# Kernel optimization log

Hardware: AMD Instinct MI355X
Metric: run time of the kernel (lower is better)

## Reference

```python
import jax, jax.numpy as jnp
import numpy as np

D = 512
HEADS, DIM_HEAD, LANDMARKS, PINV_ITERS = 8, 64, 256, 6
CONV_K = 33  # residual depthwise conv kernel over sequence dim


def _ln(x, g, b, eps=1e-5):
    mu = x.mean(-1, keepdims=True)
    var = ((x - mu) ** 2).mean(-1, keepdims=True)
    return (x - mu) / jnp.sqrt(var + eps) * g + b


def _moe(x, gw, gb, f1w, f1b, l1g, l1b, f2w, f2b, l2g, l2b, k):
    # Dense grouped-expert evaluation (same math as per-token dispatch in torch source).
    scores = x @ gw + gb                               # [B,N,E]
    topk_s, topk_i = jax.lax.top_k(scores, k)          # [B,N,k]
    h = jnp.einsum('bnd,edh->benh', x, f1w) + f1b[None, :, None, :]
    h = jax.nn.relu(_ln(h, l1g[None, :, None, :], l1b[None, :, None, :]))
    o = jnp.einsum('benh,ehd->bend', h, f2w) + f2b[None, :, None, :]
    o = _ln(o, l2g[None, :, None, :], l2b[None, :, None, :])  # [B,E,N,D]
    o = jnp.take_along_axis(jnp.swapaxes(o, 1, 2), topk_i[..., None], axis=2)  # [B,N,k,D]
    w = jax.nn.softmax(topk_s, axis=-1)[..., None]
    return (w * o).sum(axis=2) + x


def _pinv(x, iters):
    # Moore-Penrose iterative pseudoinverse (lucidrains nystrom-attention)
    col = jnp.abs(x).sum(-1).max()
    row = jnp.abs(x).sum(-2).max()
    z = jnp.swapaxes(x, -1, -2) / (col * row)
    I = jnp.eye(x.shape[-1], dtype=x.dtype)
    for _ in range(iters):
        xz = x @ z
        z = 0.25 * z @ (13 * I - xz @ (15 * I - xz @ (7 * I - xz)))
    return z


def _nystrom(x, qkv_w, out_w, out_b, conv_w):
    b, n, _ = x.shape
    m, h, dh = LANDMARKS, HEADS, DIM_HEAD
    pad = (m - n % m) % m
    x = jnp.pad(x, ((0, 0), (pad, 0), (0, 0)))  # pad at FRONT, as in source
    npd = n + pad
    qkv = x @ qkv_w                              # [b, npd, 3*h*dh]
    q, k, v = [t.reshape(b, npd, h, dh).transpose(0, 2, 1, 3) for t in jnp.split(qkv, 3, axis=-1)]
    q = q * dh ** -0.5
    l = npd // m
    q_l = q.reshape(b, h, m, l, dh).mean(3)      # landmark means
    k_l = k.reshape(b, h, m, l, dh).mean(3)
    attn1 = jax.nn.softmax(jnp.einsum('bhid,bhjd->bhij', q, k_l), -1)    # [b,h,npd,m]
    attn2 = jax.nn.softmax(jnp.einsum('bhid,bhjd->bhij', q_l, k_l), -1)  # [b,h,m,m]
    attn3 = jax.nn.softmax(jnp.einsum('bhid,bhjd->bhij', q_l, k), -1)    # [b,h,m,npd]
    out = (attn1 @ _pinv(attn2, PINV_ITERS)) @ (attn3 @ v)               # [b,h,npd,dh]
    res = jax.lax.conv_general_dilated(
        v, conv_w, (1, 1), [(CONV_K // 2, CONV_K // 2), (0, 0)],
        dimension_numbers=('NCHW', 'OIHW', 'NCHW'), feature_group_count=h)
    out = out + res
    out = out.transpose(0, 2, 1, 3).reshape(b, npd, h * dh)
    out = out @ out_w + out_b
    return out[:, -n:]


def setup_inputs() -> dict:
    key = jax.random.key(0)
    ks = iter(jax.random.split(key, 64))
    def rn(shape, s=0.02):
        return jax.random.normal(next(ks), shape, jnp.float32) * s
    inp = {'features': jax.random.normal(next(ks), (4, 6000, D), jnp.float32)}
    inp['cls_token'] = rn((1, 1, D), 1e-6)
    def moe_params(pfx, E):
        inp[pfx + '_gate_w'] = rn((D, E)); inp[pfx + '_gate_b'] = jnp.zeros((E,), jnp.float32)
        inp[pfx + '_fc1_w'] = rn((E, D, D)); inp[pfx + '_fc1_b'] = jnp.zeros((E, D), jnp.float32)
        inp[pfx + '_ln1_g'] = jnp.ones((E, D), jnp.float32); inp[pfx + '_ln1_b'] = jnp.zeros((E, D), jnp.float32)
        inp[pfx + '_fc2_w'] = rn((E, D, D)); inp[pfx + '_fc2_b'] = jnp.zeros((E, D), jnp.float32)
        inp[pfx + '_ln2_g'] = jnp.ones((E, D), jnp.float32); inp[pfx + '_ln2_b'] = jnp.zeros((E, D), jnp.float32)
    moe_params('moe1', 2)
    moe_params('moe2', 4)
    def layer_params(pfx):
        inp[pfx + '_norm_g'] = jnp.ones((D,), jnp.float32); inp[pfx + '_norm_b'] = jnp.zeros((D,), jnp.float32)
        inp[pfx + '_qkv_w'] = rn((D, 3 * HEADS * DIM_HEAD))
        inp[pfx + '_out_w'] = rn((HEADS * DIM_HEAD, D)); inp[pfx + '_out_b'] = jnp.zeros((D,), jnp.float32)
        inp[pfx + '_conv_w'] = rn((HEADS, 1, CONV_K, 1))
    layer_params('l1')
    layer_params('l2')
    return inp


def reference(features, cls_token,
              moe1_gate_w, moe1_gate_b, moe1_fc1_w, moe1_fc1_b, moe1_ln1_g, moe1_ln1_b, moe1_fc2_w, moe1_fc2_b, moe1_ln2_g, moe1_ln2_b,
              moe2_gate_w, moe2_gate_b, moe2_fc1_w, moe2_fc1_b, moe2_ln1_g, moe2_ln1_b, moe2_fc2_w, moe2_fc2_b, moe2_ln2_g, moe2_ln2_b,
              l1_norm_g, l1_norm_b, l1_qkv_w, l1_out_w, l1_out_b, l1_conv_w,
              l2_norm_g, l2_norm_b, l2_qkv_w, l2_out_w, l2_out_b, l2_conv_w):
    B, N, _ = features.shape
    _H = int(np.ceil(np.sqrt(N)))
    add = _H * _H - N
    h = jnp.concatenate([features, features[:, :add]], axis=1)      # square pad by wrap
    h = jnp.concatenate([jnp.broadcast_to(cls_token, (B, 1, D)), h], axis=1)
    h = _moe(h, moe1_gate_w, moe1_gate_b, moe1_fc1_w, moe1_fc1_b, moe1_ln1_g, moe1_ln1_b, moe1_fc2_w, moe1_fc2_b, moe1_ln2_g, moe1_ln2_b, k=1)
    h = h + _nystrom(_ln(h, l1_norm_g, l1_norm_b), l1_qkv_w, l1_out_w, l1_out_b, l1_conv_w)
    h = _moe(h, moe2_gate_w, moe2_gate_b, moe2_fc1_w, moe2_fc1_b, moe2_ln1_g, moe2_ln1_b, moe2_fc2_w, moe2_fc2_b, moe2_ln2_g, moe2_ln2_b, k=2)
    h = h + _nystrom(_ln(h, l2_norm_g, l2_norm_b), l2_qkv_w, l2_out_w, l2_out_b, l2_conv_w)
    return (h[:, 0], h[:, 1:])
```

## Files before the change

### kernel.cpp

```cpp
#include <hip/hip_runtime.h>
#include <hip/hip_bf16.h>

constexpr int BATCH = 4;
constexpr int NTOK  = 6085;
constexpr int BN_TOK = BATCH * NTOK;
constexpr int NPD   = 6144;
constexpr int RPAD  = BATCH * NPD;
constexpr int DMODEL = 512;
constexpr int NH = 8, DH = 64;
constexpr int NBH = BATCH * NH;
constexpr int LGRP = NPD / 256;
constexpr int PAD_FRONT = 59;
constexpr int CONVK = 33;
constexpr int NCH = 8;

typedef __attribute__((ext_vector_type(8))) short short8v;
typedef __attribute__((ext_vector_type(4))) float f32x4;

__device__ __forceinline__ unsigned short f2bf(float f) {
  unsigned u = __float_as_uint(f);
  u += 0x7FFF + ((u >> 16) & 1);
  return (unsigned short)(u >> 16);
}
__device__ __forceinline__ float bf2f(unsigned short h) {
  return __uint_as_float((unsigned)h << 16);
}


__global__ void k_build_h(const float* __restrict__ feat, const float* __restrict__ cls,
                          float* __restrict__ H) {
  size_t total = (size_t)BN_TOK * DMODEL;
  for (size_t idx = (size_t)blockIdx.x * blockDim.x + threadIdx.x; idx < total;
       idx += (size_t)gridDim.x * blockDim.x) {
    int d = (int)(idx & 511);
    size_t tok = idx >> 9;
    int b = (int)(tok / NTOK), n = (int)(tok % NTOK);
    float v;
    if (n == 0) v = cls[d];
    else {
      int i = n - 1; if (i >= 6000) i -= 6000;
      v = feat[((size_t)b * 6000 + i) * DMODEL + d];
    }
    H[idx] = v;
  }
}

__global__ void k_diag_fill(float* __restrict__ out, size_t n, float val) {
  for (size_t i = (size_t)blockIdx.x * blockDim.x + threadIdx.x; i < n;
       i += (size_t)gridDim.x * blockDim.x)
    out[i] = val;
}

__global__ __launch_bounds__(256) void k_wconv(const float* __restrict__ W, int ldb,
    unsigned short* __restrict__ hi, unsigned short* __restrict__ lo) {
  __shared__ unsigned short Th[64][80], Tl[64][80];
  int bk = blockIdx.y * 64, bn = blockIdx.x * 64;
  int t = threadIdx.x;
  int kr = t >> 2, cq = (t & 3) * 16;
  const float* src = W + (size_t)(bk + kr) * ldb + bn + cq;
  #pragma unroll
  for (int q = 0; q < 4; ++q) {
    float4 v = *(const float4*)(src + q * 4);
    float vs[4] = {v.x, v.y, v.z, v.w};
    #pragma unroll
    for (int e = 0; e < 4; ++e) {
      int n = cq + q * 4 + e;
      unsigned short h = f2bf(vs[e]);
      Th[n][kr] = h;
      Tl[n][kr] = f2bf(vs[e] - bf2f(h));
    }
  }
  __syncthreads();
  int nr = t >> 2, kq = (t & 3) * 16;
  size_t o = (size_t)(bn + nr) * 512 + bk + kq;
  *(short8v*)&hi[o]     = *(const short8v*)&Th[nr][kq];
  *(short8v*)&hi[o + 8] = *(const short8v*)&Th[nr][kq + 8];
  *(short8v*)&lo[o]     = *(const short8v*)&Tl[nr][kq];
  *(short8v*)&lo[o + 8] = *(const short8v*)&Tl[nr][kq + 8];
}

__global__ __launch_bounds__(256) void k_gemm_mfma(const float* __restrict__ A,
    const unsigned short* __restrict__ BtH, const unsigned short* __restrict__ BtL,
    const float* __restrict__ bias, float* __restrict__ C,
    int M, int lda, int ldc, float alpha, int omode)
{
  __shared__ unsigned short AsH[128][40], AsL[128][40];
  __shared__ unsigned short BsH[128][40], BsL[128][40];
  int bm = blockIdx.y * 128, bn = blockIdx.x * 128;
  int tid = threadIdx.x;
  int wave = tid >> 6, lane = tid & 63;
  int mo = (wave >> 1) * 64, no = (wave & 1) * 64;
  int r16 = lane & 15, g = lane >> 4;
  f32x4 acc[4][4] = {};
  int srow = tid >> 1, shalf = (tid & 1) * 16;
  const float* aptr = A + (size_t)(bm + srow) * lda + shalf;
  bool avalid = (bm + srow) < M;
  const unsigned short* bhptr = BtH + (size_t)(bn + srow) * 512 + shalf;
  const unsigned short* blptr = BtL + (size_t)(bn + srow) * 512 + shalf;
  for (int k0 = 0; k0 < 512; k0 += 32) {
    unsigned short h8[16], l8[16];
    #pragma unroll
    for (int q = 0; q < 4; ++q) {
      float4 v = avalid ? *(const float4*)(aptr + k0 + q * 4) : make_float4(0.f, 0.f, 0.f, 0.f);
      float vs[4] = {v.x, v.y, v.z, v.w};
      #pragma unroll
      for (int e = 0; e < 4; ++e) {
        unsigned short hh = f2bf(vs[e]);
        h8[q * 4 + e] = hh;
        l8[q * 4 + e] = f2bf(vs[e] - bf2f(hh));
      }
    }
    *(short8v*)&AsH[srow][shalf]     = *(short8v*)&h8[0];
    *(short8v*)&AsH[srow][shalf + 8] = *(short8v*)&h8[8];
    *(short8v*)&AsL[srow][shalf]     = *(short8v*)&l8[0];
    *(short8v*)&AsL[srow][shalf + 8] = *(short8v*)&l8[8];
    *(short8v*)&BsH[srow][shalf]     = *(const short8v*)(bhptr + k0);
    *(short8v*)&BsH[srow][shalf + 8] = *(const short8v*)(bhptr + k0 + 8);
    *(short8v*)&BsL[srow][shalf]     = *(const short8v*)(blptr + k0);
    *(short8v*)&BsL[srow][shalf + 8] = *(const short8v*)(blptr + k0 + 8);
    __syncthreads();
    short8v ah[4], al[4], bh[4], bl[4];
    #pragma unroll
    for (int mt = 0; mt < 4; ++mt) {
      ah[mt] = *(const short8v*)&AsH[mo + mt * 16 + r16][g * 8];
      al[mt] = *(const short8v*)&AsL[mo + mt * 16 + r16][g * 8];
    }
    #pragma unroll
    for (int nt = 0; nt < 4; ++nt) {
      bh[nt] = *(const short8v*)&BsH[no + nt * 16 + r16][g * 8];
      bl[nt] = *(const short8v*)&BsL[no + nt * 16 + r16][g * 8];
    }
    #pragma unroll
    for (int mt = 0; mt < 4; ++mt)
      #pragma unroll
      for (int nt = 0; nt < 4; ++nt) {
        acc[mt][nt] = __builtin_amdgcn_mfma_f32_16x16x32_bf16(ah[mt], bh[nt], acc[mt][nt], 0, 0, 0);
        acc[mt][nt] = __builtin_amdgcn_mfma_f32_16x16x32_bf16(ah[mt], bl[nt], acc[mt][nt], 0, 0, 0);
        acc[mt][nt] = __builtin_amdgcn_mfma_f32_16x16x32_bf16(al[mt], bh[nt], acc[mt][nt], 0, 0, 0);
      }
    __syncthreads();
  }
  #pragma unroll
  for (int mt = 0; mt < 4; ++mt)
    #pragma unroll
    for (int nt = 0; nt < 4; ++nt)
      #pragma unroll
      for (int j = 0; j < 4; ++j) {
        int gr = bm + mo + mt * 16 + g * 4 + j;
        int gc = bn + no + nt * 16 + r16;
        if (gr >= M) continue;
        float v = alpha * acc[mt][nt][j] + (bias ? bias[gc] : 0.f);
        if (omode == 0) {
          C[(size_t)gr * ldc + gc] = v;
        } else if (omode == 2) {
          int bb = gr / NPD, ii = gr % NPD;
          if (ii >= PAD_FRONT)
            C[((size_t)bb * NTOK + ii - PAD_FRONT) * 512 + gc] += v;
        } else {
          int bb = gr / NPD, ii = gr % NPD;
          int hh = gc >> 6, dd = gc & 63;
          C[(((size_t)bb * NH + hh) * NPD + ii) * 64 + dd] = v;
        }
      }
}

__global__ __launch_bounds__(256) void k_gemm(const float* __restrict__ A,
    const float* __restrict__ B,
    const float* __restrict__ bias, float* __restrict__ C,
    int M, int N, int K, int lda, int ldb, int ldc,
    long long sA, long long sB, long long sC, float alpha, int omode, float cdiag)
{
  __shared__ float As[16][65];
  __shared__ float Bs[16][65];
  int z = blockIdx.z;
  A += (size_t)z * (size_t)sA;
  B += (size_t)z * (size_t)sB;
  int bm = blockIdx.y * 64, bn = blockIdx.x * 64;
  int tid = threadIdx.x;
  int tr = tid >> 4, tc = tid & 15;
  int ar = tid >> 2, aq = tid & 3;
  int br = tid >> 4, bq = tid & 15;
  float acc[4][4] = {};
  for (int k0 = 0; k0 < K; k0 += 16) {
    {
      int gr = bm + ar;
      float4 v = make_float4(0.f, 0.f, 0.f, 0.f);
      if (gr < M) v = *(const float4*)&A[(size_t)gr * lda + k0 + aq * 4];
      As[aq * 4 + 0][ar] = v.x; As[aq * 4 + 1][ar] = v.y;
      As[aq * 4 + 2][ar] = v.z; As[aq * 4 + 3][ar] = v.w;
    }
    {
      float4 v = *(const float4*)&B[(size_t)(k0 + br) * ldb + bn + bq * 4];
      Bs[br][bq * 4 + 0] = v.x; Bs[br][bq * 4 + 1] = v.y;
      Bs[br][bq * 4 + 2] = v.z; Bs[br][bq * 4 + 3] = v.w;
    }
    __syncthreads();
    #pragma unroll
    for (int kk = 0; kk < 16; ++kk) {
      float a[4], bv[4];
      #pragma unroll
      for (int i = 0; i < 4; ++i) a[i] = As[kk][tr * 4 + i];
      #pragma unroll
      for (int j = 0; j < 4; ++j) bv[j] = Bs[kk][tc * 4 + j];
      #pragma unroll
      for (int i = 0; i < 4; ++i)
        #pragma unroll
        for (int j = 0; j < 4; ++j) acc[i][j] += a[i] * bv[j];
    }
    __syncthreads();
  }
  #pragma unroll
  for (int i = 0; i < 4; ++i) {
    int gr = bm + tr * 4 + i;
    if (gr >= M) continue;
    #pragma unroll
    for (int j = 0; j < 4; ++j) {
      int gc = bn + tc * 4 + j;
      float v;
      if (omode == 5) {
        v = ((gr == gc) ? cdiag : 0.f) - acc[i][j];
      } else {
        v = alpha * acc[i][j] + (bias ? bias[gc] : 0.f);
      }
      C[(size_t)z * (size_t)sC + (size_t)gr * ldc + gc] = v;
    }
  }
}

__global__ void k_gate(const float* __restrict__ X, const float* __restrict__ gw,
                       const float* __restrict__ gb, float* __restrict__ WT, int E, int k) {
  int tok = blockIdx.x; int lane = threadIdx.x;
  const float* x = X + (size_t)tok * DMODEL;
  float s[4] = {0.f, 0.f, 0.f, 0.f};
  for (int d = lane; d < DMODEL; d += 64) {
    float xv = x[d];
    for (int e = 0; e < E; ++e) s[e] += xv * gw[(size_t)d * E + e];
  }
  #pragma unroll
  for (int off = 32; off; off >>= 1) {
    #pragma unroll
    for (int e = 0; e < 4; ++e) s[e] += __shfl_down(s[e], off);
  }
  if (lane == 0) {
    for (int e = 0; e < E; ++e) s[e] += gb[e];
    float w[4] = {0.f, 0.f, 0.f, 0.f};
    int i1 = 0;
    for (int e = 1; e < E; ++e) if (s[e] > s[i1]) i1 = e;
    if (k == 1) {
      w[i1] = 1.f;
    } else {
      int i2 = -1;
      for (int e = 0; e < E; ++e) { if (e == i1) continue; if (i2 < 0 || s[e] > s[i2]) i2 = e; }
      float e2 = expf(s[i2] - s[i1]);
      float zz = 1.f + e2;
      w[i1] = 1.f / zz; w[i2] = e2 / zz;
    }
    #pragma unroll
    for (int e = 0; e < 4; ++e) WT[(size_t)tok * 4 + e] = w[e];
  }
}

__device__ __forceinline__ void wave_ln_stats(const float* x, int lane, float& mu, float& rstd) {
  float s = 0.f, q = 0.f;
  #pragma unroll
  for (int j = 0; j < 8; ++j) { float v = x[lane + 64 * j]; s += v; q += v * v; }
  #pragma unroll
  for (int off = 32; off; off >>= 1) { s += __shfl_xor(s, off); q += __shfl_xor(q, off); }
  mu = s * (1.f / 512.f);
  float var = q * (1.f / 512.f) - mu * mu;
  rstd = rsqrtf(var + 1e-5f);
}

__global__ void k_ln_relu(float* __restrict__ T, const float* __restrict__ g,
                          const float* __restrict__ b) {
  int row = blockIdx.x; int lane = threadIdx.x;
  float* x = T + (size_t)row * 512;
  float mu, rstd; wave_ln_stats(x, lane, mu, rstd);
  #pragma unroll
  for (int j = 0; j < 8; ++j) {
    int d = lane + 64 * j;
    float v = (x[d] - mu) * rstd * g[d] + b[d];
    x[d] = fmaxf(v, 0.f);
  }
}

__global__ void k_ln_waccum(const float* __restrict__ T, float* __restrict__ H,
                            const float* __restrict__ g, const float* __restrict__ b,
                            const float* __restrict__ WT, int e) {
  int row = blockIdx.x;
  float w = WT[(size_t)row * 4 + e];
  if (w == 0.f) return;
  int lane = threadIdx.x;
  const float* x = T + (size_t)row * 512;
  float mu, rstd; wave_ln_stats(x, lane, mu, rstd);
  float* h = H + (size_t)row * 512;
  #pragma unroll
  for (int j = 0; j < 8; ++j) {
    int d = lane + 64 * j;
    h[d] += w * ((x[d] - mu) * rstd * g[d] + b[d]);
  }
}

__global__ void k_ln_pad(const float* __restrict__ H, float* __restrict__ XLn,
                         const float* __restrict__ g, const float* __restrict__ b) {
  int row = blockIdx.x; int lane = threadIdx.x;
  int bb = row / NPD, i = row % NPD;
  float* y = XLn + (size_t)row * 512;
  if (i < PAD_FRONT) {
    #pragma unroll
    for (int j = 0; j < 8; ++j) y[lane + 64 * j] = 0.f;
    return;
  }
  const float* x = H + ((size_t)bb * NTOK + (i - PAD_FRONT)) * 512;
  float mu, rstd; wave_ln_stats(x, lane, mu, rstd);
  #pragma unroll
  for (int j = 0; j < 8; ++j) {
    int d = lane + 64 * j;
    y[d] = (x[d] - mu) * rstd * g[d] + b[d];
  }
}

__global__ void k_xmean(const float* __restrict__ XLn, float* __restrict__ Xm) {
  int z = blockIdx.x;
  int c = threadIdx.x;
  int b = z >> 8, jm = z & 255;
  const float* base = XLn + ((size_t)b * NPD + jm * LGRP) * 512 + c;
  float s = 0.f;
  #pragma unroll
  for (int t = 0; t < LGRP; ++t) s += base[(size_t)t * 512];
  Xm[(size_t)z * 512 + c] = s * (1.f / LGRP);
}

__global__ __launch_bounds__(256) void k_attn2(const float* __restrict__ QL,
                                               const float* __restrict__ KL,
                                               float* __restrict__ A2) {
  int z = blockIdx.x; int bh = z >> 8, j = z & 255;
  int b = bh >> 3, h = bh & 7;
  int t = threadIdx.x;
  __shared__ float q[64]; __shared__ float red[256];
  __shared__ float mshare, sshare;
  if (t < 64) q[t] = QL[((size_t)b * 256 + j) * 512 + h * 64 + t];
  __syncthreads();
  const float* kl = KL + ((size_t)b * 256 + t) * 512 + h * 64;
  float s = 0.f;
  #pragma unroll
  for (int d = 0; d < 64; ++d) s += q[d] * kl[d];
  red[t] = s; __syncthreads();
  for (int st = 128; st; st >>= 1) { if (t < st) red[t] = fmaxf(red[t], red[t + st]); __syncthreads(); }
  if (t == 0) mshare = red[0];
  __syncthreads();
  float e = expf(s - mshare);
  red[t] = e; __syncthreads();
  for (int st = 128; st; st >>= 1) { if (t < st) red[t] += red[t + st]; __syncthreads(); }
  if (t == 0) sshare = red[0];
  __syncthreads();
  A2[((size_t)bh * 256 + j) * 256 + t] = e / sshare;
}

__global__ __launch_bounds__(256) void k_pinv_scalars(const float* __restrict__ A2,
                                                      unsigned int* __restrict__ sc) {
  int bh = blockIdx.x; int t = threadIdx.x;
  const float* A = A2 + (size_t)bh * 65536;
  float rowsum = 0.f, colsum = 0.f;
  for (int jj = 0; jj < 256; ++jj) {
    rowsum += fabsf(A[(size_t)t * 256 + jj]);
    colsum += fabsf(A[(size_t)jj * 256 + t]);
  }
  __shared__ float sh[256];
  sh[t] = rowsum; __syncthreads();
  for (int s = 128; s; s >>= 1) { if (t < s) sh[t] = fmaxf(sh[t], sh[t + s]); __syncthreads(); }
  if (t == 0) atomicMax(&sc[0], __float_as_uint(sh[0]));
  __syncthreads();
  sh[t] = colsum; __syncthreads();
  for (int s = 128; s; s >>= 1) { if (t < s) sh[t] = fmaxf(sh[t], sh[t + s]); __syncthreads(); }
  if (t == 0) atomicMax(&sc[1], __float_as_uint(sh[0]));
}

__global__ void k_zinit(const float* __restrict__ A2, float* __restrict__ Z,
                        const unsigned int* __restrict__ sc) {
  float scale = 1.f / (__uint_as_float(sc[0]) * __uint_as_float(sc[1]));
  size_t total = (size_t)NBH * 65536;
  for (size_t idx = (size_t)blockIdx.x * blockDim.x + threadIdx.x; idx < total;
       idx += (size_t)gridDim.x * blockDim.x) {
    size_t bh = idx >> 16; int r = (int)((idx >> 8) & 255); int cc = (int)(idx & 255);
    Z[idx] = A2[(bh << 16) + (size_t)cc * 256 + r] * scale;
  }
}

__global__ void k_diagsub(const float* __restrict__ in, float* __restrict__ out, float cdiag) {
  size_t total = (size_t)NBH * 65536;
  for (size_t idx = (size_t)blockIdx.x * blockDim.x + threadIdx.x; idx < total;
       idx += (size_t)gridDim.x * blockDim.x) {
    int r = (int)((idx >> 8) & 255); int cc = (int)(idx & 255);
    out[idx] = ((r == cc) ? cdiag : 0.f) - in[idx];
  }
}

__global__ __launch_bounds__(256) void k_flash_mfma(
    const float* __restrict__ Qp, long long Qsb, long long Qsh, int Qsr,
    const float* __restrict__ Kp, long long Ksb, long long Ksh, int Ksr,
    const float* __restrict__ Vp, long long Vsb, long long Vsh, int Vsr,
    float* __restrict__ Op, long long Osb, long long Osh, int Osr,
    float* __restrict__ Opart, float* __restrict__ ML,
    int tiles_per_chunk, int mode)
{
  int jt = blockIdx.x, bh = blockIdx.y, ch = blockIdx.z;
  int b = bh >> 3, h = bh & 7;
  const float* Qb = Qp + (size_t)b * Qsb + (size_t)h * Qsh;
  const float* Kb = Kp + (size_t)b * Ksb + (size_t)h * Ksh;
  const float* Vb = Vp + (size_t)b * Vsb + (size_t)h * Vsh;
  int tid = threadIdx.x;
  int wave = tid >> 6, lane = tid & 63;
  int r16 = lane & 15, g = lane >> 4;
  int q0 = jt * 64 + wave * 16;

  __shared__ unsigned short KsH[64][72], KsL[64][72];
  __shared__ unsigned short VtH[64][72], VtL[64][72];

  short8v qh[2], ql[2];
  #pragma unroll
  for (int kk = 0; kk < 2; ++kk) {
    const float* qr = Qb + (size_t)(q0 + r16) * Qsr + kk * 32 + g * 8;
    float4 v0 = *(const float4*)qr;
    float4 v1 = *(const float4*)(qr + 4);
    float vs[8] = {v0.x, v0.y, v0.z, v0.w, v1.x, v1.y, v1.z, v1.w};
    unsigned short hh[8], llo[8];
    #pragma unroll
    for (int e = 0; e < 8; ++e) {
      hh[e] = f2bf(vs[e]); llo[e] = f2bf(vs[e] - bf2f(hh[e]));
    }
    qh[kk] = *(short8v*)&hh[0];
    ql[kk] = *(short8v*)&llo[0];
  }

  f32x4 O4[4] = {};
  float m[4], lsum[4];
  #pragma unroll
  for (int j = 0; j < 4; ++j) { m[j] = -1e30f; lsum[j] = 0.f; }

  int skey = tid >> 2, sq = (tid & 3) * 16;
  int t0 = ch * tiles_per_chunk;
  for (int tt = t0; tt < t0 + tiles_per_chunk; ++tt) {
    int key0 = tt * 64;
    __syncthreads();
    {
      const float* krow = Kb + (size_t)(key0 + skey) * Ksr + sq;
      const float* vrow = Vb + (size_t)(key0 + skey) * Vsr + sq;
      #pragma unroll
      for (int q = 0; q < 4; ++q) {
        float4 kv = *(const float4*)(krow + q * 4);
        float4 vv = *(const float4*)(vrow + q * 4);
        float ks[4] = {kv.x, kv.y, kv.z, kv.w};
        float vvs[4] = {vv.x, vv.y, vv.z, vv.w};
        #pragma unroll
        for (int e = 0; e < 4; ++e) {
          int d = sq + q * 4 + e;
          unsigned short khh = f2bf(ks[e]);
          KsH[skey][d] = khh;
          KsL[skey][d] = f2bf(ks[e] - bf2f(khh));
          unsigned short vhh = f2bf(vvs[e]);
          VtH[d][skey] = vhh;
          VtL[d][skey] = f2bf(vvs[e] - bf2f(vhh));
        }
      }
    }
    __syncthreads();
    f32x4 S[4] = {};
    #pragma unroll
    for (int kk = 0; kk < 2; ++kk)
      #pragma unroll
      for (int nt = 0; nt < 4; ++nt) {
        short8v kh = *(const short8v*)&KsH[nt * 16 + r16][kk * 32 + g * 8];
        short8v kl = *(const short8v*)&KsL[nt * 16 + r16][kk * 32 + g * 8];
        S[nt] = __builtin_amdgcn_mfma_f32_16x16x32_bf16(qh[kk], kh, S[nt], 0, 0, 0);
        S[nt] = __builtin_amdgcn_mfma_f32_16x16x32_bf16(qh[kk], kl, S[nt], 0, 0, 0);
        S[nt] = __builtin_amdgcn_mfma_f32_16x16x32_bf16(ql[kk], kh, S[nt], 0, 0, 0);
      }
    float tmax[4];
    #pragma unroll
    for (int j = 0; j < 4; ++j)
      tmax[j] = fmaxf(fmaxf(S[0][j], S[1][j]), fmaxf(S[2][j], S[3][j]));
    #pragma unroll
    for (int off = 8; off; off >>= 1)
      #pragma unroll
      for (int j = 0; j < 4; ++j) tmax[j] = fmaxf(tmax[j], __shfl_xor(tmax[j], off));
    float corr[4];
    #pragma unroll
    for (int j = 0; j < 4; ++j) {
      float mn = fmaxf(m[j], tmax[j]);
      corr[j] = expf(m[j] - mn);
      m[j] = mn;
    }
    __syncthreads();
    float tl[4] = {0.f, 0.f, 0.f, 0.f};
    #pragma unroll
    for (int nt = 0; nt < 4; ++nt)
      #pragma unroll
      for (int j = 0; j < 4; ++j) {
        float p = expf(S[nt][j] - m[j]);
        tl[j] += p;
        unsigned short ph = f2bf(p);
        KsH[wave * 16 + g * 4 + j][nt * 16 + r16] = ph;
        KsL[wave * 16 + g * 4 + j][nt * 16 + r16] = f2bf(p - bf2f(ph));
      }
    #pragma unroll
    for (int off = 8; off; off >>= 1)
      #pragma unroll
      for (int j = 0; j < 4; ++j) tl[j] += __shfl_xor(tl[j], off);
    #pragma unroll
    for (int j = 0; j < 4; ++j) lsum[j] = lsum[j] * corr[j] + tl[j];
    #pragma unroll
    for (int nt = 0; nt < 4; ++nt)
      #pragma unroll
      for (int j = 0; j < 4; ++j) O4[nt][j] *= corr[j];
    #pragma unroll
    for (int kk = 0; kk < 2; ++kk) {
      short8v ph = *(const short8v*)&KsH[wave * 16 + r16][kk * 32 + g * 8];
      short8v pl = *(const short8v*)&KsL[wave * 16 + r16][kk * 32 + g * 8];
      #pragma unroll
      for (int nt = 0; nt < 4; ++nt) {
        short8v vh = *(const short8v*)&VtH[nt * 16 + r16][kk * 32 + g * 8];
        short8v vl = *(const short8v*)&VtL[nt * 16 + r16][kk * 32 + g * 8];
        O4[nt] = __builtin_amdgcn_mfma_f32_16x16x32_bf16(ph, vh, O4[nt], 0, 0, 0);
        O4[nt] = __builtin_amdgcn_mfma_f32_16x16x32_bf16(ph, vl, O4[nt], 0, 0, 0);
        O4[nt] = __builtin_amdgcn_mfma_f32_16x16x32_bf16(pl, vh, O4[nt], 0, 0, 0);
      }
    }
  }
  if (mode == 0) {
    float* Ob = Op + (size_t)b * Osb + (size_t)h * Osh;
    float inv[4];
    #pragma unroll
    for (int j = 0; j < 4; ++j) inv[j] = 1.f / lsum[j];
    #pragma unroll
    for (int nt = 0; nt < 4; ++nt)
      #pragma unroll
      for (int j = 0; j < 4; ++j)
        Ob[(size_t)(q0 + g * 4 + j) * Osr + nt * 16 + r16] = O4[nt][j] * inv[j];
  } else {
    #pragma unroll
    for (int j = 0; j < 4; ++j) {
      size_t rowbase = ((size_t)ch * NBH + bh) * 256 + q0 + g * 4 + j;
      #pragma unroll
      for (int nt = 0; nt < 4; ++nt)
        Opart[rowbase * 64 + nt * 16 + r16] = O4[nt][j];
      if (r16 == 0) { ML[rowbase * 2] = m[j]; ML[rowbase * 2 + 1] = lsum[j]; }
    }
  }
}

__global__ __launch_bounds__(256) void k_flash_comb(const float* __restrict__ Opart,
                                                    const float* __restrict__ ML,
                                                    float* __restrict__ A3V) {
  int jt = blockIdx.x, bh = blockIdx.y;
  int t = threadIdx.x;
  int jr = t >> 4, q16 = t & 15;
  int row = jt * 16 + jr;
  float mv[NCH], lv[NCH];
  float M = -1e30f;
  #pragma unroll
  for (int ch = 0; ch < NCH; ++ch) {
    size_t base = (((size_t)ch * NBH + bh) * 256 + row);
    mv[ch] = ML[base * 2]; lv[ch] = ML[base * 2 + 1];
    M = fmaxf(M, mv[ch]);
  }
  float L = 0.f;
  float4 O = make_float4(0.f, 0.f, 0.f, 0.f);
  #pragma unroll
  for (int ch = 0; ch < NCH; ++ch) {
    float c = expf(mv[ch] - M);
    L += c * lv[ch];
    size_t base = (((size_t)ch * NBH + bh) * 256 + row);
    float4 o = *(const float4*)&Opart[base * 64 + q16 * 4];
    O.x += c * o.x; O.y += c * o.y; O.z += c * o.z; O.w += c * o.w;
  }
  float inv = 1.f / L;
  *(float4*)&A3V[((size_t)bh * 256 + row) * 64 + q16 * 4] =
      make_float4(O.x * inv, O.y * inv, O.z * inv, O.w * inv);
}

__global__ void k_conv_add(const float* __restrict__ Vp, const float* __restrict__ cw,
                           float* __restrict__ out) {
  int row = blockIdx.x; int c = threadIdx.x;
  int b = row / NPD, i = row % NPD;
  int h = c >> 6, d = c & 63;
  const float* vb = Vp + ((size_t)(b * NH + h) * NPD) * 64 + d;
  float acc = 0.f;
  #pragma unroll
  for (int tp = 0; tp < CONVK; ++tp) {
    int ii = i + tp - CONVK / 2;
    if (ii >= 0 && ii < NPD)
      acc += cw[h * CONVK + tp] * vb[(size_t)ii * 64];
  }
  out[(size_t)row * 512 + c] += acc;
}

__global__ void k_out_write(const float* __restrict__ H, float* __restrict__ out) {
  size_t n0 = (size_t)BATCH * 512;
  size_t total = n0 + (size_t)BATCH * (NTOK - 1) * 512;
  for (size_t idx = (size_t)blockIdx.x * blockDim.x + threadIdx.x; idx < total;
       idx += (size_t)gridDim.x * blockDim.x) {
    float v;
    if (idx < n0) {
      int b = (int)(idx >> 9); int d = (int)(idx & 511);
      v = H[((size_t)b * NTOK) * 512 + d];
    } else {
      size_t r = idx - n0;
      size_t bj = r >> 9; int d = (int)(r & 511);
      int b = (int)(bj / (NTOK - 1)); int j = (int)(bj % (NTOK - 1));
      v = H[((size_t)b * NTOK + 1 + j) * 512 + d];
    }
    out[idx] = v;
  }
}


extern "C" void kernel_launch(void* const* d_in, const int* in_sizes, int n_in,
                              void* d_out, int out_size, void* d_ws, size_t ws_size,
                              hipStream_t stream) {
  (void)in_sizes; (void)n_in;

  const float* feat = (const float*)d_in[0];
  const float* cls  = (const float*)d_in[1];
  const float* m1_gw = (const float*)d_in[2];  const float* m1_gb = (const float*)d_in[3];
  const float* m1_f1w = (const float*)d_in[4]; const float* m1_f1b = (const float*)d_in[5];
  const float* m1_l1g = (const float*)d_in[6]; const float* m1_l1b = (const float*)d_in[7];
  const float* m1_f2w = (const float*)d_in[8]; const float* m1_f2b = (const float*)d_in[9];
  const float* m1_l2g = (const float*)d_in[10]; const float* m1_l2b = (const float*)d_in[11];
  const float* m2_gw = (const float*)d_in[12]; const float* m2_gb = (const float*)d_in[13];
  const float* m2_f1w = (const float*)d_in[14]; const float* m2_f1b = (const float*)d_in[15];
  const float* m2_l1g = (const float*)d_in[16]; const float* m2_l1b = (const float*)d_in[17];
  const float* m2_f2w = (const float*)d_in[18]; const float* m2_f2b = (const float*)d_in[19];
  const float* m2_l2g = (const float*)d_in[20]; const float* m2_l2b = (const float*)d_in[21];
  const float* l1_ng = (const float*)d_in[22]; const float* l1_nb = (const float*)d_in[23];
  const float* l1_qkvw = (const float*)d_in[24]; const float* l1_outw = (const float*)d_in[25];
  const float* l1_outb = (const float*)d_in[26]; const float* l1_convw = (const float*)d_in[27];
  const float* l2_ng = (const float*)d_in[28]; const float* l2_nb = (const float*)d_in[29];
  const float* l2_qkvw = (const float*)d_in[30]; const float* l2_outw = (const float*)d_in[31];
  const float* l2_outb = (const float*)d_in[32]; const float* l2_convw = (const float*)d_in[33];

  constexpr size_t SZ_H    = (size_t)BN_TOK * 512;
  constexpr size_t SZ_ROW  = (size_t)RPAD * 512;
  float* W = (float*)d_ws;
  float* H  = W;
  float* WT = W + SZ_H;
  unsigned int* SC = (unsigned int*)(W + SZ_H + 97360);
  float* pool = W + SZ_H + 97360 + 16;

  float* R2 = pool;
  float* R3 = pool + SZ_ROW;
  float* R4 = pool + 2 * SZ_ROW;
  float* SMALL = pool + 3 * SZ_ROW;
  float* Xm  = SMALL;
  float* QL  = SMALL + 524288;
  float* KL  = SMALL + 1048576;
  float* A2  = SMALL + 1572864;
  float* Zb  = SMALL + 3670016;
  float* XZ  = SMALL + 5767168;
  float* Wa  = SMALL + 7864320;
  float* Wb  = SMALL + 9961472;
  float* A3V = SMALL + 12058624;
  float* W2b = SMALL + 12582912;
  size_t total_f = (SZ_H + 97360 + 16) + 3 * SZ_ROW + 13107200;
  if (total_f * 4 > ws_size) {
    k_diag_fill<<<2048, 256, 0, stream>>>((float*)d_out, (size_t)out_size,
                                          (float)(ws_size >> 20));
    return;
  }

  k_build_h<<<2048, 256, 0, stream>>>(feat, cls, H);

  auto run_moe = [&](const float* gw, const float* gb, const float* f1w, const float* f1b,
                     const float* l1g, const float* l1b, const float* f2w, const float* f2b,
                     const float* l2g, const float* l2b, int E, int k) {
    float* T1 = R2; float* T2 = R3; float* Xsnap = R4;
    unsigned short* BtHi = (unsigned short*)A2;
    unsigned short* BtLo = (unsigned short*)(A2 + 131072);
    hipMemcpyAsync(Xsnap, H, SZ_H * 4, hipMemcpyDeviceToDevice, stream);
    k_gate<<<BN_TOK, 64, 0, stream>>>(H, gw, gb, WT, E, k);
    dim3 g(4, (BN_TOK + 127) / 128, 1);
    for (int e = 0; e < E; ++e) {
      k_wconv<<<dim3(8, 8), 256, 0, stream>>>(f1w + (size_t)e * 262144, 512, BtHi, BtLo);
      k_gemm_mfma<<<g, 256, 0, stream>>>(Xsnap, BtHi, BtLo, f1b + e * 512, T1,
          BN_TOK, 512, 512, 1.f, 0);
      k_ln_relu<<<BN_TOK, 64, 0, stream>>>(T1, l1g + e * 512, l1b + e * 512);
      k_wconv<<<dim3(8, 8), 256, 0, stream>>>(f2w + (size_t)e * 262144, 512, BtHi, BtLo);
      k_gemm_mfma<<<g, 256, 0, stream>>>(T1, BtHi, BtLo, f2b + e * 512, T2,
          BN_TOK, 512, 512, 1.f, 0);
      k_ln_waccum<<<BN_TOK, 64, 0, stream>>>(T2, H, l2g + e * 512, l2b + e * 512, WT, e);
    }
  };

  auto run_attn = [&](const float* ng, const float* nb, const float* qkvw, const float* outw,
                      const float* outb, const float* convw) {
    float* XLn = R2; float* AttnO = R2;
    float* Kp = R3; float* Qb = R3; float* Vp = R4;
    k_ln_pad<<<RPAD, 64, 0, stream>>>(H, XLn, ng, nb);
    k_xmean<<<BATCH * 256, 512, 0, stream>>>(XLn, Xm);
    k_gemm<<<dim3(8, 16, 1), 256, 0, stream>>>(Xm, qkvw, nullptr, QL,
        1024, 512, 512, 512, 1536, 512, 0, 0, 0, 0.125f, 0, 0.f);
    k_gemm<<<dim3(8, 16, 1), 256, 0, stream>>>(Xm, qkvw + 512, nullptr, KL,
        1024, 512, 512, 512, 1536, 512, 0, 0, 0, 1.f, 0, 0.f);
    k_attn2<<<NBH * 256, 256, 0, stream>>>(QL, KL, A2);
    hipMemsetAsync(SC, 0, 8, stream);
    k_pinv_scalars<<<NBH, 256, 0, stream>>>(A2, SC);
    k_zinit<<<2048, 256, 0, stream>>>(A2, Zb, SC);
    float* zp = Zb; float* wp = Wb;
    dim3 gp(4, 4, NBH);
    for (int it = 0; it < 6; ++it) {
      k_gemm<<<gp, 256, 0, stream>>>(A2, zp, nullptr, XZ,
          256, 256, 256, 256, 256, 256, 65536, 65536, 65536, 1.f, 0, 0.f);
      k_diagsub<<<2048, 256, 0, stream>>>(XZ, Wa, 7.f);
      k_gemm<<<gp, 256, 0, stream>>>(XZ, Wa, nullptr, wp,
          256, 256, 256, 256, 256, 256, 65536, 65536, 65536, 1.f, 5, 15.f);
      k_gemm<<<gp, 256, 0, stream>>>(XZ, wp, nullptr, Wa,
          256, 256, 256, 256, 256, 256, 65536, 65536, 65536, 1.f, 5, 13.f);
      k_gemm<<<gp, 256, 0, stream>>>(zp, Wa, nullptr, wp,
          256, 256, 256, 256, 256, 256, 65536, 65536, 65536, 0.25f, 0, 0.f);
      float* tsw = zp; zp = wp; wp = tsw;
    }
    unsigned short* BtQH = (unsigned short*)XZ;
    unsigned short* BtQL = (unsigned short*)(XZ + 393216);
    k_wconv<<<dim3(24, 8), 256, 0, stream>>>(qkvw, 1536, BtQH, BtQL);
    dim3 gr(4, (RPAD + 127) / 128, 1);
    k_gemm_mfma<<<gr, 256, 0, stream>>>(XLn, BtQH + 512 * 512, BtQL + 512 * 512, nullptr,
        Kp, RPAD, 512, 512, 1.f, 3);
    k_gemm_mfma<<<gr, 256, 0, stream>>>(XLn, BtQH + 1024 * 512, BtQL + 1024 * 512, nullptr,
        Vp, RPAD, 512, 512, 1.f, 3);
    k_flash_mfma<<<dim3(4, NBH, NCH), 256, 0, stream>>>(
        QL, 131072LL, 64LL, 512,
        Kp, (long long)NH * NPD * 64, (long long)NPD * 64, 64,
        Vp, (long long)NH * NPD * 64, (long long)NPD * 64, 64,
        nullptr, 0, 0, 0, Wa, Xm, NPD / (64 * NCH), 1);
    k_flash_comb<<<dim3(16, NBH), 256, 0, stream>>>(Wa, Xm, A3V);
    k_gemm<<<dim3(1, 4, NBH), 256, 0, stream>>>(zp, A3V, nullptr, W2b,
        256, 64, 256, 256, 64, 64, 65536, 16384, 16384, 1.f, 0, 0.f);
    k_gemm_mfma<<<gr, 256, 0, stream>>>(XLn, BtQH, BtQL, nullptr,
        Qb, RPAD, 512, 512, 0.125f, 0);
    k_flash_mfma<<<dim3(NPD / 64, NBH, 1), 256, 0, stream>>>(
        Qb, (long long)NPD * 512, 64LL, 512,
        KL, 131072LL, 64LL, 512,
        W2b, 131072LL, 16384LL, 64,
        AttnO, (long long)NPD * 512, 64LL, 512,
        nullptr, nullptr, 256 / 64, 0);
    k_conv_add<<<RPAD, 512, 0, stream>>>(Vp, convw, AttnO);
    unsigned short* BtOH = (unsigned short*)Wa;
    unsigned short* BtOL = (unsigned short*)(Wa + 131072);
    k_wconv<<<dim3(8, 8), 256, 0, stream>>>(outw, 512, BtOH, BtOL);
    k_gemm_mfma<<<gr, 256, 0, stream>>>(AttnO, BtOH, BtOL, outb,
        H, RPAD, 512, 512, 1.f, 2);
  };

  run_moe(m1_gw, m1_gb, m1_f1w, m1_f1b, m1_l1g, m1_l1b, m1_f2w, m1_f2b, m1_l2g, m1_l2b, 2, 1);
  run_attn(l1_ng, l1_nb, l1_qkvw, l1_outw, l1_outb, l1_convw);
  run_moe(m2_gw, m2_gb, m2_f1w, m2_f1b, m2_l1g, m2_l1b, m2_f2w, m2_f2b, m2_l2g, m2_l2b, 4, 2);
  run_attn(l2_ng, l2_nb, l2_qkvw, l2_outw, l2_outb, l2_convw);

  k_out_write<<<2048, 256, 0, stream>>>(H, (float*)d_out);
}
```

Measured before the change: 4.279 ms.

## Move pinv iterations to split-bf16 MFMA GEMM, tile depthwise conv through LDS

```diff
diff --git a/kernel.cpp b/kernel.cpp
--- a/kernel.cpp
+++ b/kernel.cpp
@@ -12,7 +12,7 @@
 constexpr int LGRP = NPD / 256;
 constexpr int PAD_FRONT = 59;
 constexpr int CONVK = 33;
-constexpr int NCH = 8;
+constexpr int NCH = 4;
 
 typedef __attribute__((ext_vector_type(8))) short short8v;
 typedef __attribute__((ext_vector_type(4))) float f32x4;
@@ -162,6 +162,124 @@
           C[(((size_t)bb * NH + hh) * NPD + ii) * 64 + dd] = v;
         }
       }
+}
+
+__global__ __launch_bounds__(256) void k_gemm_mfma2(const float* __restrict__ A,
+    const float* __restrict__ Bt, float* __restrict__ C,
+    float alpha, int omode, float cdiag, int premap)
+{
+  __shared__ unsigned short AsH[128][40], AsL[128][40];
+  __shared__ unsigned short BsH[128][40], BsL[128][40];
+  size_t zo = (size_t)blockIdx.z * 65536;
+  int bm = blockIdx.y * 128, bn = blockIdx.x * 128;
+  int tid = threadIdx.x;
+  int wave = tid >> 6, lane = tid & 63;
+  int mo = (wave >> 1) * 64, no = (wave & 1) * 64;
+  int r16 = lane & 15, g = lane >> 4;
+  f32x4 acc[4][4] = {};
+  int srow = tid >> 1, shalf = (tid & 1) * 16;
+  int grow = bm + srow;
+  int gn = bn + srow;
+  for (int k0 = 0; k0 < 256; k0 += 32) {
+    unsigned short h8[16], l8[16];
+    #pragma unroll
+    for (int q = 0; q < 4; ++q) {
+      float4 v = *(const float4*)&A[zo + (size_t)grow * 256 + k0 + shalf + q * 4];
+      float vs[4] = {v.x, v.y, v.z, v.w};
+      #pragma unroll
+      for (int e = 0; e < 4; ++e) {
+        float a = vs[e];
+        if (premap) a = ((grow == (k0 + shalf + q * 4 + e)) ? 7.f : 0.f) - a;
+        unsigned short hh = f2bf(a);
+        h8[q * 4 + e] = hh;
+        l8[q * 4 + e] = f2bf(a - bf2f(hh));
+      }
+    }
+    *(short8v*)&AsH[srow][shalf]     = *(short8v*)&h8[0];
+    *(short8v*)&AsH[srow][shalf + 8] = *(short8v*)&h8[8];
+    *(short8v*)&AsL[srow][shalf]     = *(short8v*)&l8[0];
+    *(short8v*)&AsL[srow][shalf + 8] = *(short8v*)&l8[8];
+    #pragma unroll
+    for (int q = 0; q < 4; ++q) {
+      float4 v = *(const float4*)&Bt[zo + (size_t)gn * 256 + k0 + shalf + q * 4];
+      float vs[4] = {v.x, v.y, v.z, v.w};
+      #pragma unroll
+      for (int e = 0; e < 4; ++e) {
+        unsigned short hh = f2bf(vs[e]);
+        h8[q * 4 + e] = hh;
+        l8[q * 4 + e] = f2bf(vs[e] - bf2f(hh));
+      }
+    }
+    *(short8v*)&BsH[srow][shalf]     = *(short8v*)&h8[0];
+    *(short8v*)&BsH[srow][shalf + 8] = *(short8v*)&h8[8];
+    *(short8v*)&BsL[srow][shalf]     = *(short8v*)&l8[0];
+    *(short8v*)&BsL[srow][shalf + 8] = *(short8v*)&l8[8];
+    __syncthreads();
+    short8v ah[4], al[4], bh[4], bl[4];
+    #pragma unroll
+    for (int mt = 0; mt < 4; ++mt) {
+      ah[mt] = *(const short8v*)&AsH[mo + mt * 16 + r16][g * 8];
+      al[mt] = *(const short8v*)&AsL[mo + mt * 16 + r16][g * 8];
+    }
+    #pragma unroll
+    for (int nt = 0; nt < 4; ++nt) {
+      bh[nt] = *(const short8v*)&BsH[no + nt * 16 + r16][g * 8];
+      bl[nt] = *(const short8v*)&BsL[no + nt * 16 + r16][g * 8];
+    }
+    #pragma unroll
+    for (int mt = 0; mt < 4; ++mt)
+      #pragma unroll
+      for (int nt = 0; nt < 4; ++nt) {
+        acc[mt][nt] = __builtin_amdgcn_mfma_f32_16x16x32_bf16(ah[mt], bh[nt], acc[mt][nt], 0, 0, 0);
+        acc[mt][nt] = __builtin_amdgcn_mfma_f32_16x16x32_bf16(ah[mt], bl[nt], acc[mt][nt], 0, 0, 0);
+        acc[mt][nt] = __builtin_amdgcn_mfma_f32_16x16x32_bf16(al[mt], bh[nt], acc[mt][nt], 0, 0, 0);
+      }
+    __syncthreads();
+  }
+  #pragma unroll
+  for (int mt = 0; mt < 4; ++mt)
+    #pragma unroll
+    for (int nt = 0; nt < 4; ++nt)
+      #pragma unroll
+      for (int j = 0; j < 4; ++j) {
+        int gr = bm + mo + mt * 16 + g * 4 + j;
+        int gc = bn + no + nt * 16 + r16;
+        float v;
+        if (omode == 5) v = ((gr == gc) ? cdiag : 0.f) - acc[mt][nt][j];
+        else            v = alpha * acc[mt][nt][j];
+        C[zo + (size_t)gr * 256 + gc] = v;
+      }
+}
+
+__global__ __launch_bounds__(256) void k_tpose(const float* __restrict__ in,
+                                               float* __restrict__ out) {
+  __shared__ float Ts[64][65];
+  int bx = blockIdx.x * 64, by = blockIdx.y * 64;
+  size_t zo = (size_t)blockIdx.z * 65536;
+  int t = threadIdx.x;
+  int r = t >> 4, c4 = (t & 15) * 4;
+  #pragma unroll
+  for (int u = 0; u < 4; ++u) {
+    float4 v = *(const float4*)&in[zo + (size_t)(by + r + u * 16) * 256 + bx + c4];
+    Ts[r + u * 16][c4 + 0] = v.x; Ts[r + u * 16][c4 + 1] = v.y;
+    Ts[r + u * 16][c4 + 2] = v.z; Ts[r + u * 16][c4 + 3] = v.w;
+  }
+  __syncthreads();
+  #pragma unroll
+  for (int u = 0; u < 4; ++u) {
+    int rr = r + u * 16;
+    float4 v = make_float4(Ts[c4][rr], Ts[c4 + 1][rr], Ts[c4 + 2][rr], Ts[c4 + 3][rr]);
+    *(float4*)&out[zo + (size_t)(bx + rr) * 256 + by + c4] = v;
+  }
+}
+
+__global__ void k_y0(const float* __restrict__ A2, float* __restrict__ Y,
+                     const unsigned int* __restrict__ sc) {
+  float scale = 1.f / (__uint_as_float(sc[0]) * __uint_as_float(sc[1]));
+  size_t total = (size_t)NBH * 65536;
+  for (size_t idx = (size_t)blockIdx.x * blockDim.x + threadIdx.x; idx < total;
+       idx += (size_t)gridDim.x * blockDim.x)
+    Y[idx] = A2[idx] * scale;
 }
 
 __global__ __launch_bounds__(256) void k_gemm(const float* __restrict__ A,
@@ -387,15 +505,6 @@
   }
 }
 
-__global__ void k_diagsub(const float* __restrict__ in, float* __restrict__ out, float cdiag) {
-  size_t total = (size_t)NBH * 65536;
-  for (size_t idx = (size_t)blockIdx.x * blockDim.x + threadIdx.x; idx < total;
-       idx += (size_t)gridDim.x * blockDim.x) {
-    int r = (int)((idx >> 8) & 255); int cc = (int)(idx & 255);
-    out[idx] = ((r == cc) ? cdiag : 0.f) - in[idx];
-  }
-}
-
 __global__ __launch_bounds__(256) void k_flash_mfma(
     const float* __restrict__ Qp, long long Qsb, long long Qsh, int Qsr,
     const float* __restrict__ Kp, long long Ksb, long long Ksh, int Ksr,
@@ -579,20 +688,35 @@
       make_float4(O.x * inv, O.y * inv, O.z * inv, O.w * inv);
 }
 
-__global__ void k_conv_add(const float* __restrict__ Vp, const float* __restrict__ cw,
-                           float* __restrict__ out) {
-  int row = blockIdx.x; int c = threadIdx.x;
-  int b = row / NPD, i = row % NPD;
-  int h = c >> 6, d = c & 63;
-  const float* vb = Vp + ((size_t)(b * NH + h) * NPD) * 64 + d;
-  float acc = 0.f;
-  #pragma unroll
-  for (int tp = 0; tp < CONVK; ++tp) {
-    int ii = i + tp - CONVK / 2;
-    if (ii >= 0 && ii < NPD)
-      acc += cw[h * CONVK + tp] * vb[(size_t)ii * 64];
-  }
-  out[(size_t)row * 512 + c] += acc;
+__global__ __launch_bounds__(256) void k_conv_add(const float* __restrict__ Vp,
+                                                  const float* __restrict__ cw,
+                                                  float* __restrict__ out) {
+  int it = blockIdx.x, bh = blockIdx.y;
+  int b = bh >> 3, h = bh & 7;
+  int i0 = it * 128;
+  int t = threadIdx.x;
+  __shared__ float Vs[160][64];
+  const float* vb = Vp + (size_t)bh * NPD * 64;
+  #pragma unroll
+  for (int u = 0; u < 10; ++u) {
+    int idx = t + 256 * u;
+    int r = idx >> 4, c4 = (idx & 15) * 4;
+    int gi = i0 - 16 + r;
+    float4 v = make_float4(0.f, 0.f, 0.f, 0.f);
+    if (gi >= 0 && gi < NPD) v = *(const float4*)&vb[(size_t)gi * 64 + c4];
+    *(float4*)&Vs[r][c4] = v;
+  }
+  __syncthreads();
+  float w[CONVK];
+  #pragma unroll
+  for (int p = 0; p < CONVK; ++p) w[p] = cw[h * CONVK + p];
+  int wave = t >> 6, d = t & 63;
+  for (int rr = wave * 32; rr < wave * 32 + 32; ++rr) {
+    float acc = 0.f;
+    #pragma unroll
+    for (int p = 0; p < CONVK; ++p) acc += w[p] * Vs[rr + p][d];
+    out[((size_t)b * NPD + i0 + rr) * 512 + h * 64 + d] += acc;
+  }
 }
 
 __global__ void k_out_write(const float* __restrict__ H, float* __restrict__ out) {
@@ -704,23 +828,22 @@
     k_attn2<<<NBH * 256, 256, 0, stream>>>(QL, KL, A2);
     hipMemsetAsync(SC, 0, 8, stream);
     k_pinv_scalars<<<NBH, 256, 0, stream>>>(A2, SC);
-    k_zinit<<<2048, 256, 0, stream>>>(A2, Zb, SC);
-    float* zp = Zb; float* wp = Wb;
-    dim3 gp(4, 4, NBH);
+    k_y0<<<2048, 256, 0, stream>>>(A2, Zb, SC);
+    k_zinit<<<2048, 256, 0, stream>>>(A2, Wb, SC);
+    float* Y = Zb; float* Z = Wb; float* F1 = XZ; float* F2 = Wa;
+    dim3 gq(2, 2, NBH);
     for (int it = 0; it < 6; ++it) {
-      k_gemm<<<gp, 256, 0, stream>>>(A2, zp, nullptr, XZ,
-          256, 256, 256, 256, 256, 256, 65536, 65536, 65536, 1.f, 0, 0.f);
-      k_diagsub<<<2048, 256, 0, stream>>>(XZ, Wa, 7.f);
-      k_gemm<<<gp, 256, 0, stream>>>(XZ, Wa, nullptr, wp,
-          256, 256, 256, 256, 256, 256, 65536, 65536, 65536, 1.f, 5, 15.f);
-      k_gemm<<<gp, 256, 0, stream>>>(XZ, wp, nullptr, Wa,
-          256, 256, 256, 256, 256, 256, 65536, 65536, 65536, 1.f, 5, 13.f);
-      k_gemm<<<gp, 256, 0, stream>>>(zp, Wa, nullptr, wp,
-          256, 256, 256, 256, 256, 256, 65536, 65536, 65536, 0.25f, 0, 0.f);
-      float* tsw = zp; zp = wp; wp = tsw;
-    }
-    unsigned short* BtQH = (unsigned short*)XZ;
-    unsigned short* BtQL = (unsigned short*)(XZ + 393216);
+      k_gemm_mfma2<<<gq, 256, 0, stream>>>(Y, A2, F1, 1.f, 0, 0.f, 0);
+      k_gemm_mfma2<<<gq, 256, 0, stream>>>(A2, Y, F2, 1.f, 0, 0.f, 0);
+      k_gemm_mfma2<<<gq, 256, 0, stream>>>(F1, F2, Y, 1.f, 5, 15.f, 1);
+      k_gemm_mfma2<<<gq, 256, 0, stream>>>(Y, F2, F1, 1.f, 5, 13.f, 0);
+      k_gemm_mfma2<<<gq, 256, 0, stream>>>(Z, F1, F2, 0.25f, 0, 0.f, 0);
+      float* tz = Z; Z = F2; F2 = tz;
+      if (it < 5)
+        k_tpose<<<dim3(4, 4, NBH), 256, 0, stream>>>(Z, Y);
+    }
+    unsigned short* BtQH = (unsigned short*)Wa;
+    unsigned short* BtQL = (unsigned short*)(Wa + 393216);
     k_wconv<<<dim3(24, 8), 256, 0, stream>>>(qkvw, 1536, BtQH, BtQL);
     dim3 gr(4, (RPAD + 127) / 128, 1);
     k_gemm_mfma<<<gr, 256, 0, stream>>>(XLn, BtQH + 512 * 512, BtQL + 512 * 512, nullptr,
@@ -731,9 +854,9 @@
         QL, 131072LL, 64LL, 512,
         Kp, (long long)NH * NPD * 64, (long long)NPD * 64, 64,
         Vp, (long long)NH * NPD * 64, (long long)NPD * 64, 64,
-        nullptr, 0, 0, 0, Wa, Xm, NPD / (64 * NCH), 1);
-    k_flash_comb<<<dim3(16, NBH), 256, 0, stream>>>(Wa, Xm, A3V);
-    k_gemm<<<dim3(1, 4, NBH), 256, 0, stream>>>(zp, A3V, nullptr, W2b,
+        nullptr, 0, 0, 0, XZ, Xm, NPD / (64 * NCH), 1);
+    k_flash_comb<<<dim3(16, NBH), 256, 0, stream>>>(XZ, Xm, A3V);
+    k_gemm<<<dim3(1, 4, NBH), 256, 0, stream>>>(Z, A3V, nullptr, W2b,
         256, 64, 256, 256, 64, 64, 65536, 16384, 16384, 1.f, 0, 0.f);
     k_gemm_mfma<<<gr, 256, 0, stream>>>(XLn, BtQH, BtQL, nullptr,
         Qb, RPAD, 512, 512, 0.125f, 0);
@@ -743,7 +866,7 @@
         W2b, 131072LL, 16384LL, 64,
         AttnO, (long long)NPD * 512, 64LL, 512,
         nullptr, nullptr, 256 / 64, 0);
-    k_conv_add<<<RPAD, 512, 0, stream>>>(Vp, convw, AttnO);
+    k_conv_add<<<dim3(NPD / 128, NBH), 256, 0, stream>>>(Vp, convw, AttnO);
     unsigned short* BtOH = (unsigned short*)Wa;
     unsigned short* BtOL = (unsigned short*)(Wa + 131072);
     k_wconv<<<dim3(8, 8), 256, 0, stream>>>(outw, 512, BtOH, BtOL);
```

After: 3.734 ms. 1.15x faster.
